# Kernel optimization log

Hardware: AMD Instinct MI355X
Metric: run time of the kernel (lower is better)

## Reference

```python
import jax, jax.numpy as jnp
import numpy as np

B, S, V, L, H, NH, NL = 4, 256, 64, 10, 128, 8, 3
DH = H // NH
LP1 = L + 1


def setup_inputs() -> dict:
    key = jax.random.key(0)
    ks = jax.random.split(key, 18)
    sc = 1.0 / np.sqrt(H)
    return {
        "x": jax.random.normal(ks[0], (B, S, V), jnp.float32),
        "adjacency_logits": jax.random.normal(ks[1], (V, V, LP1), jnp.float32) * 0.1,
        "var_emb": jax.random.normal(ks[2], (V, H), jnp.float32),
        "temp_emb": jax.random.normal(ks[3], (LP1, H), jnp.float32),
        "mech_W": jax.random.normal(ks[4], (V, NL, H, H), jnp.float32) * sc,
        "mech_b": jax.random.normal(ks[5], (V, NL, H), jnp.float32) * 0.01,
        "ln_g": jnp.ones((V, NL, H), jnp.float32),
        "ln_b": jnp.zeros((V, NL, H), jnp.float32),
        "Wq": jax.random.normal(ks[6], (V, H, H), jnp.float32) * sc,
        "Wk": jax.random.normal(ks[7], (V, H, H), jnp.float32) * sc,
        "Wv": jax.random.normal(ks[8], (V, H, H), jnp.float32) * sc,
        "Wo": jax.random.normal(ks[9], (V, H, H), jnp.float32) * sc,
        "bq": jnp.zeros((V, H), jnp.float32),
        "bk": jnp.zeros((V, H), jnp.float32),
        "bv": jnp.zeros((V, H), jnp.float32),
        "bo": jnp.zeros((V, H), jnp.float32),
        "out_W": jax.random.normal(ks[10], (V, H), jnp.float32) * sc,
        "out_b": jnp.zeros((V,), jnp.float32),
    }


def reference(x, adjacency_logits, var_emb, temp_emb, mech_W, mech_b, ln_g, ln_b,
              Wq, Wk, Wv, Wo, bq, bk, bv, bo, out_W, out_b):
    b, s, v = x.shape
    lp1 = adjacency_logits.shape[-1]
    adj = jax.nn.sigmoid(adjacency_logits)  # (V_src, V_tgt, L+1), soft adjacency

    # xlag[b,t,src,l] = x[b, t-l, src] with zero padding (the shift-pad loop, fused)
    xlag = jnp.stack([jnp.pad(x, ((0, 0), (l, 0), (0, 0)))[:, :s] for l in range(lp1)], axis=-1)

    # causal_input[b,t,tgt,h] = sum_{src,l} xlag * adj[src,tgt,l] * (var_emb[src,h] + temp_emb[l,h])
    A = jnp.einsum('btsl,sil->btis', xlag, adj)   # contracted over lag
    Bl = jnp.einsum('btsl,sil->btil', xlag, adj)  # contracted over source
    z = jnp.einsum('btis,sh->btih', A, var_emb) + jnp.einsum('btil,lh->btih', Bl, temp_emb)  # (B,S,V,H)

    # per-variable causal mechanism: Linear -> LayerNorm -> GELU (dropout = identity at eval)
    eps = 1e-5
    nl = mech_W.shape[1]
    for li in range(nl):
        z = jnp.einsum('btvh,vhk->btvk', z, mech_W[:, li]) + mech_b[:, li]
        mu = z.mean(axis=-1, keepdims=True)
        var = z.var(axis=-1, keepdims=True)
        z = (z - mu) / jnp.sqrt(var + eps) * ln_g[:, li] + ln_b[:, li]
        z = jax.nn.gelu(z, approximate=False)

    # per-variable multi-head self-attention over the sequence axis
    def heads(t):
        return t.reshape(b, s, v, NH, DH)
    q = heads(jnp.einsum('btvh,vhk->btvk', z, Wq) + bq)
    k = heads(jnp.einsum('btvh,vhk->btvk', z, Wk) + bk)
    vv = heads(jnp.einsum('btvh,vhk->btvk', z, Wv) + bv)
    scores = jnp.einsum('bqvnd,bkvnd->bvnqk', q, k) / np.sqrt(DH)  # (B,V,NH,S,S)
    attn = jax.nn.softmax(scores, axis=-1)
    o = jnp.einsum('bvnqk,bkvnd->bqvnd', attn, vv).reshape(b, s, v, NH * DH)
    o = jnp.einsum('btvh,vhk->btvk', o, Wo) + bo

    # per-variable output head Linear(H, 1), concatenated over variables
    predictions = jnp.einsum('btvh,vh->btv', o, out_W) + out_b  # (B,S,V)
    return predictions
```

## Files before the change

### kernel.cpp

```cpp
#include <hip/hip_runtime.h>
#include <math.h>

#define BB   4
#define SS   256
#define VV   64
#define LP1  11
#define HH   128
#define NHH  8
#define DHH  16
#define NLL  3
#define BSZ  1024

typedef unsigned short u16;
typedef unsigned int   u32;
typedef __attribute__((ext_vector_type(8))) short s16x8;
typedef __attribute__((ext_vector_type(4))) float f32x4;

__device__ __forceinline__ float bfbits2f(u32 hi16) {
    u32 i = hi16 << 16; float f; __builtin_memcpy(&f, &i, 4); return f;
}
__device__ __forceinline__ u16 f2bf(float f) {
    u32 i; __builtin_memcpy(&i, &f, 4);
    return (u16)((i + 0x7fffu + ((i >> 16) & 1u)) >> 16);
}
__device__ __forceinline__ u16 f2bf_trunc(float f) {
    u32 i; __builtin_memcpy(&i, &f, 4);
    return (u16)(i >> 16);
}
__device__ __forceinline__ float ldf(const void* p, size_t i, int isbf) {
    if (isbf) return bfbits2f(((const u16*)p)[i]);
    return ((const float*)p)[i];
}
__device__ __forceinline__ float4 ld4(const void* p, size_t i, int isbf) {
    float4 v;
    if (isbf) {
        uint2 u = *(const uint2*)((const u16*)p + i);
        v.x = bfbits2f(u.x & 0xffffu); v.y = bfbits2f(u.x >> 16);
        v.z = bfbits2f(u.y & 0xffffu); v.w = bfbits2f(u.y >> 16);
    } else {
        v = *(const float4*)((const float*)p + i);
    }
    return v;
}

__global__ __launch_bounds__(64) void k_sniff(const u16* __restrict__ probe,
                                              int* __restrict__ flags) {
    if (threadIdx.x == 0) {
        int wild = 0;
        for (int j = 0; j < 256; j++) {
            float v = bfbits2f(probe[j]);
            if (!(fabsf(v) < 1e8f)) wild = 1;
        }
        flags[0] = wild ? 0 : 1;
    }
}

__global__ __launch_bounds__(256) void k_adj(const void* __restrict__ logits,
                                             float* __restrict__ adj,
                                             const int* __restrict__ flags) {
    int isbf = flags[0];
    int i = blockIdx.x * 256 + threadIdx.x;
    if (i < VV * VV * LP1) {
        float v = ldf(logits, i, isbf);
        adj[i] = 1.f / (1.f + expf(-v));
    }
}

__global__ __launch_bounds__(128) void k_fuse(const void* __restrict__ Wo,
                                              const void* __restrict__ outW,
                                              const void* __restrict__ bo,
                                              const void* __restrict__ outb,
                                              float* __restrict__ wfused,
                                              float* __restrict__ bfused,
                                              const int* __restrict__ flags) {
    int isbf = flags[0];
    int v = blockIdx.x; int h = threadIdx.x;
    __shared__ float ow[HH];
    __shared__ float red[HH];
    ow[h] = ldf(outW, (size_t)v * HH + h, isbf);
    __syncthreads();
    size_t wb = ((size_t)v * HH + h) * HH;
    float acc = 0.f;
    #pragma unroll 8
    for (int k = 0; k < HH; k++) acc += ldf(Wo, wb + k, isbf) * ow[k];
    wfused[v * HH + h] = acc;
    red[h] = ldf(bo, (size_t)v * HH + h, isbf) * ow[h];
    __syncthreads();
    for (int s = 64; s > 0; s >>= 1) { if (h < s) red[h] += red[h + s]; __syncthreads(); }
    if (h == 0) bfused[v] = red[0] + ldf(outb, v, isbf);
}

__global__ __launch_bounds__(256) void k_causal(const void* __restrict__ x,
                                                const float* __restrict__ adj,
                                                const void* __restrict__ var_emb,
                                                const void* __restrict__ temp_emb,
                                                u16* __restrict__ zh,
                                                u16* __restrict__ zl,
                                                const int* __restrict__ flags) {
    __shared__ float xl[LP1][VV];
    __shared__ float A_sh[VV][VV + 1];
    __shared__ float Blp_sh[VV * LP1 * 4];
    __shared__ float Bl_sh[VV][12];
    int isbf = flags[0];
    int tid = threadIdx.x;
    int bt = blockIdx.x; int b = bt >> 8; int t = bt & 255;

    for (int p = tid; p < LP1 * VV; p += 256) {
        int l = p >> 6, s = p & 63; int tt = t - l;
        xl[l][s] = (tt >= 0) ? ldf(x, (size_t)(b * SS + tt) * VV + s, isbf) : 0.f;
    }
    __syncthreads();

    {
        int i = tid & 63, sg = tid >> 6;
        float blp[LP1];
        #pragma unroll
        for (int l = 0; l < LP1; l++) blp[l] = 0.f;
        for (int k = 0; k < 16; k++) {
            int s = sg + k * 4;
            const float* ap = adj + (s * VV + i) * LP1;
            float a = 0.f;
            #pragma unroll
            for (int l = 0; l < LP1; l++) {
                float pr = xl[l][s] * ap[l];
                a += pr; blp[l] += pr;
            }
            A_sh[i][s] = a;
        }
        #pragma unroll
        for (int l = 0; l < LP1; l++)
            Blp_sh[(i * LP1 + l) * 4 + sg] = blp[l];
    }
    __syncthreads();
    for (int p = tid; p < VV * LP1; p += 256) {
        int i = p / LP1, l = p - i * LP1;
        const float* q = &Blp_sh[(i * LP1 + l) * 4];
        Bl_sh[i][l] = (q[0] + q[1]) + (q[2] + q[3]);
    }
    __syncthreads();

    int h0 = (tid & 31) * 4;
    int ig = tid >> 5;
    float acc[8][4];
    #pragma unroll
    for (int ii = 0; ii < 8; ii++)
        #pragma unroll
        for (int j = 0; j < 4; j++) acc[ii][j] = 0.f;

    if (isbf) {
        for (int s = 0; s < VV; s++) {
            float4 v4 = ld4(var_emb, (size_t)s * HH + h0, 1);
            #pragma unroll
            for (int ii = 0; ii < 8; ii++) {
                float a = A_sh[ig * 8 + ii][s];
                acc[ii][0] += a * v4.x; acc[ii][1] += a * v4.y;
                acc[ii][2] += a * v4.z; acc[ii][3] += a * v4.w;
            }
        }
        #pragma unroll
        for (int l = 0; l < LP1; l++) {
            float4 t4 = ld4(temp_emb, (size_t)l * HH + h0, 1);
            #pragma unroll
            for (int ii = 0; ii < 8; ii++) {
                float bl = Bl_sh[ig * 8 + ii][l];
                acc[ii][0] += bl * t4.x; acc[ii][1] += bl * t4.y;
                acc[ii][2] += bl * t4.z; acc[ii][3] += bl * t4.w;
            }
        }
    } else {
        for (int s = 0; s < VV; s++) {
            float4 v4 = ld4(var_emb, (size_t)s * HH + h0, 0);
            #pragma unroll
            for (int ii = 0; ii < 8; ii++) {
                float a = A_sh[ig * 8 + ii][s];
                acc[ii][0] += a * v4.x; acc[ii][1] += a * v4.y;
                acc[ii][2] += a * v4.z; acc[ii][3] += a * v4.w;
            }
        }
        #pragma unroll
        for (int l = 0; l < LP1; l++) {
            float4 t4 = ld4(temp_emb, (size_t)l * HH + h0, 0);
            #pragma unroll
            for (int ii = 0; ii < 8; ii++) {
                float bl = Bl_sh[ig * 8 + ii][l];
                acc[ii][0] += bl * t4.x; acc[ii][1] += bl * t4.y;
                acc[ii][2] += bl * t4.z; acc[ii][3] += bl * t4.w;
            }
        }
    }

    #pragma unroll
    for (int ii = 0; ii < 8; ii++) {
        int i = ig * 8 + ii;
        size_t idx = ((size_t)i * BSZ + bt) * HH + h0;
        u16 h0_ = f2bf(acc[ii][0]), h1_ = f2bf(acc[ii][1]);
        u16 h2_ = f2bf(acc[ii][2]), h3_ = f2bf(acc[ii][3]);
        uint2 hw, lw;
        hw.x = (u32)h0_ | ((u32)h1_ << 16); hw.y = (u32)h2_ | ((u32)h3_ << 16);
        lw.x = (u32)f2bf(acc[ii][0] - bfbits2f(h0_)) | ((u32)f2bf(acc[ii][1] - bfbits2f(h1_)) << 16);
        lw.y = (u32)f2bf(acc[ii][2] - bfbits2f(h2_)) | ((u32)f2bf(acc[ii][3] - bfbits2f(h3_)) << 16);
        *(uint2*)&zh[idx] = hw;
        *(uint2*)&zl[idx] = lw;
    }
}

struct WPack {
    const void* src[4];
    u16* dh[4];
    u16* dl[4];
};
#define TP 136
__global__ __launch_bounds__(256) void k_wprep(WPack wp,
                                               const int* __restrict__ flags) {
    int isbf = flags[0];
    int mat = blockIdx.x;
    int seg = (mat < 192) ? 0 : 1 + ((mat - 192) >> 6);
    int rel = (mat < 192) ? mat : ((mat - 192) & 63);
    const void* raw = wp.src[seg];
    u16* Wh = wp.dh[seg];
    u16* Wl = wp.dl[seg];
    int tid = threadIdx.x;
    size_t src = (size_t)rel * (HH * HH);
    if (isbf) {
        __shared__ u16 tile[HH * TP];
        const uint4* sp = (const uint4*)((const u16*)raw + src);
        #pragma unroll
        for (int u = 0; u < 8; u++) {
            int p = u * 256 + tid;
            int h = p >> 4, k8 = (p & 15) * 8;
            int k8s = k8 ^ ((((u32)h >> 3) & 15) * 8);
            *(uint4*)&tile[h * TP + k8s] = sp[p];
        }
        __syncthreads();
        #pragma unroll
        for (int u = 0; u < 8; u++) {
            int p = u * 256 + tid;
            int kcol = p >> 4, h8 = (p & 15) * 8;
            u16 vals[8];
            #pragma unroll
            for (int j = 0; j < 8; j++) {
                int h = h8 + j;
                int ks = kcol ^ ((((u32)h >> 3) & 15) * 8);
                vals[j] = tile[h * TP + ks];
            }
            uint4 pk;
            pk.x = (u32)vals[0] | ((u32)vals[1] << 16);
            pk.y = (u32)vals[2] | ((u32)vals[3] << 16);
            pk.z = (u32)vals[4] | ((u32)vals[5] << 16);
            pk.w = (u32)vals[6] | ((u32)vals[7] << 16);
            *(uint4*)&Wh[src + (size_t)kcol * HH + h8] = pk;
        }
    } else {
        int kcol = tid >> 1, h0 = (tid & 1) * 64;
        size_t dst = src + (size_t)kcol * HH;
        for (int i = 0; i < 64; i++) {
            int h = h0 + i;
            float w = ldf(raw, src + (size_t)h * HH + kcol, 0);
            u16 hi = f2bf(w);
            Wh[dst + h] = hi;
            Wl[dst + h] = f2bf(w - bfbits2f(hi));
        }
    }
}

#define PZ 136
#define PB 72
__global__ __launch_bounds__(256) void k_mega(
    const u16* __restrict__ zh, const u16* __restrict__ zl,
    const u16* __restrict__ WmH, const u16* __restrict__ WmL,
    const u16* __restrict__ WqH, const u16* __restrict__ WqL,
    const u16* __restrict__ WkH, const u16* __restrict__ WkL,
    const u16* __restrict__ WvH, const u16* __restrict__ WvL,
    const void* __restrict__ mechb,
    const void* __restrict__ lng, const void* __restrict__ lnb,
    const void* __restrict__ bq, const void* __restrict__ bk,
    const void* __restrict__ bv,
    u16* __restrict__ Qh, u16* __restrict__ Ql,
    u16* __restrict__ Ko, u16* __restrict__ Vt,
    const int* __restrict__ flags)
{
    __shared__ u16 Az_h[64 * PZ];
    __shared__ u16 Az_l[64 * PZ];
    __shared__ u16 Bh_s[128 * PB];
    __shared__ u16 Bl_s[128 * PB];
    int isbf = flags[0];
    int wexact = isbf;
    int tid = threadIdx.x;
    int tile = blockIdx.x, v = blockIdx.y;
    int wave = tid >> 6, lane = tid & 63;
    int quad = lane >> 4, l15 = lane & 15;
    int m0 = wave * 16;

    size_t zbase = ((size_t)v * BSZ + (size_t)tile * 64) * HH;
    #pragma unroll
    for (int u = 0; u < 4; u++) {
        int idx = u * 256 + tid;
        int row = idx >> 4, k8 = (idx & 15) * 8;
        *(uint4*)&Az_h[row * PZ + k8] = *(const uint4*)&zh[zbase + (size_t)row * HH + k8];
        *(uint4*)&Az_l[row * PZ + k8] = *(const uint4*)&zl[zbase + (size_t)row * HH + k8];
    }

    for (int li = 0; li < 6; li++) {
        const u16* Wh; const u16* Wl; size_t wbase;
        if (li < 3)       { Wh = WmH; Wl = WmL; wbase = (size_t)(v * NLL + li) * (HH * HH); }
        else if (li == 3) { Wh = WqH; Wl = WqL; wbase = (size_t)v * (HH * HH); }
        else if (li == 4) { Wh = WkH; Wl = WkL; wbase = (size_t)v * (HH * HH); }
        else              { Wh = WvH; Wl = WvL; wbase = (size_t)v * (HH * HH); }

        f32x4 acc[8];
        #pragma unroll
        for (int nt = 0; nt < 8; nt++) {
            f32x4 zz = {0.f, 0.f, 0.f, 0.f};
            acc[nt] = zz;
        }

        for (int c = 0; c < 2; c++) {
            __syncthreads();
            #pragma unroll
            for (int u = 0; u < 4; u++) {
                int p = u * 256 + tid;
                int n = p >> 3, k8 = (p & 7) * 8;
                *(uint4*)&Bh_s[n * PB + k8] =
                    *(const uint4*)&Wh[wbase + (size_t)n * HH + c * 64 + k8];
            }
            if (!wexact) {
                #pragma unroll
                for (int u = 0; u < 4; u++) {
                    int p = u * 256 + tid;
                    int n = p >> 3, k8 = (p & 7) * 8;
                    *(uint4*)&Bl_s[n * PB + k8] =
                        *(const uint4*)&Wl[wbase + (size_t)n * HH + c * 64 + k8];
                }
            }
            __syncthreads();

            #pragma unroll
            for (int kk = 0; kk < 2; kk++) {
                int ka = c * 64 + kk * 32 + quad * 8;
                int kb = kk * 32 + quad * 8;
                s16x8 ah = *(const s16x8*)&Az_h[(m0 + l15) * PZ + ka];
                s16x8 al = *(const s16x8*)&Az_l[(m0 + l15) * PZ + ka];
                if (wexact) {
                    #pragma unroll
                    for (int nt = 0; nt < 8; nt++) {
                        s16x8 bh = *(const s16x8*)&Bh_s[(nt * 16 + l15) * PB + kb];
                        acc[nt] = __builtin_amdgcn_mfma_f32_16x16x32_bf16(ah, bh, acc[nt], 0, 0, 0);
                        acc[nt] = __builtin_amdgcn_mfma_f32_16x16x32_bf16(al, bh, acc[nt], 0, 0, 0);
                    }
                } else {
                    #pragma unroll
                    for (int nt = 0; nt < 8; nt++) {
                        s16x8 bh = *(const s16x8*)&Bh_s[(nt * 16 + l15) * PB + kb];
                        s16x8 bl = *(const s16x8*)&Bl_s[(nt * 16 + l15) * PB + kb];
                        acc[nt] = __builtin_amdgcn_mfma_f32_16x16x32_bf16(ah, bh, acc[nt], 0, 0, 0);
                        acc[nt] = __builtin_amdgcn_mfma_f32_16x16x32_bf16(al, bh, acc[nt], 0, 0, 0);
                        acc[nt] = __builtin_amdgcn_mfma_f32_16x16x32_bf16(ah, bl, acc[nt], 0, 0, 0);
                    }
                }
            }
        }

        float bcol[8], gcol[8], b2col[8];
        #pragma unroll
        for (int nt = 0; nt < 8; nt++) {
            int col = nt * 16 + l15;
            if (li < 3) {
                size_t pb = (size_t)v * (NLL * HH) + (size_t)li * HH + col;
                bcol[nt]  = ldf(mechb, pb, isbf);
                gcol[nt]  = ldf(lng, pb, isbf);
                b2col[nt] = ldf(lnb, pb, isbf);
            } else {
                const void* bp = (li == 3) ? bq : (li == 4) ? bk : bv;
                bcol[nt] = ldf(bp, (size_t)v * HH + col, isbf);
            }
        }
        #pragma unroll
        for (int r = 0; r < 4; r++) {
            float vals[8];
            float sum = 0.f, sq = 0.f;
            #pragma unroll
            for (int nt = 0; nt < 8; nt++) {
                float val = acc[nt][r] + bcol[nt];
                vals[nt] = val; sum += val; sq += val * val;
            }
            int rloc = m0 + quad * 4 + r;
            if (li < 3) {
                #pragma unroll
                for (int m = 1; m < 16; m <<= 1) {
                    sum += __shfl_xor(sum, m);
                    sq  += __shfl_xor(sq, m);
                }
                float mean = sum * (1.f / HH);
                float var  = sq * (1.f / HH) - mean * mean;
                float rstd = rsqrtf(var + 1e-5f);
                #pragma unroll
                for (int nt = 0; nt < 8; nt++) {
                    float y = (vals[nt] - mean) * rstd * gcol[nt] + b2col[nt];
                    y = 0.5f * y * (1.f + erff(y * 0.70710678118654752f));
                    u16 hi = f2bf(y);
                    Az_h[rloc * PZ + nt * 16 + l15] = hi;
                    Az_l[rloc * PZ + nt * 16 + l15] = f2bf(y - bfbits2f(hi));
                }
            } else {
                int row = tile * 64 + rloc;
                size_t ob = ((size_t)v * BSZ + row) * HH;
                if (li == 3) {
                    #pragma unroll
                    for (int nt = 0; nt < 8; nt++) {
                        u16 hi = f2bf(vals[nt]);
                        Qh[ob + nt * 16 + l15] = hi;
                        Ql[ob + nt * 16 + l15] = f2bf(vals[nt] - bfbits2f(hi));
                    }
                } else if (li == 4) {
                    #pragma unroll
                    for (int nt = 0; nt < 8; nt++)
                        Ko[ob + nt * 16 + l15] = f2bf(vals[nt]);
                } else {
                    int bb = row >> 8, tt = row & 255;
                    #pragma unroll
                    for (int nt = 0; nt < 8; nt++)
                        Vt[(((size_t)(v * BB + bb) * NHH + nt) * DHH + l15) * SS + tt] = f2bf(vals[nt]);
                }
            }
        }
    }
}

#define LDW 40
__global__ __launch_bounds__(256) void k_attn2(const u16* __restrict__ Qh,
                                               const u16* __restrict__ Ql,
                                               const u16* __restrict__ K16,
                                               const u16* __restrict__ Vt,
                                               float* __restrict__ O) {
    __shared__ u16 Kp_sh[SS * LDW];
    __shared__ u16 Vt_sh[DHH * 264];
    __shared__ u16 P_sh[4][16 * LDW];
    int tid = threadIdx.x;
    int wave = tid >> 6, lane = tid & 63;
    int quad = lane >> 4, l15 = lane & 15;
    int bn = blockIdx.x, v = blockIdx.y;
    int b = bn >> 3, n = bn & 7;
    size_t qkbase = ((size_t)v * BSZ + b * SS) * HH + n * DHH;
    size_t vtbase = ((size_t)(v * BB + b) * NHH + n) * DHH * SS;

    {
        int row = tid;
        uint4 k0 = *(const uint4*)&K16[qkbase + (size_t)row * HH];
        uint4 k1 = *(const uint4*)&K16[qkbase + (size_t)row * HH + 8];
        *(uint4*)&Kp_sh[row * LDW + 0]  = k0;
        *(uint4*)&Kp_sh[row * LDW + 8]  = k1;
        *(uint4*)&Kp_sh[row * LDW + 16] = k0;
        *(uint4*)&Kp_sh[row * LDW + 24] = k1;
    }
    #pragma unroll
    for (int u = 0; u < 2; u++) {
        int p = u * 256 + tid;
        int d = p >> 5, su = (p & 31) * 8;
        *(uint4*)&Vt_sh[d * 264 + su] = *(const uint4*)&Vt[vtbase + (size_t)d * SS + su];
    }
    __syncthreads();

    s16x8 ones;
    #pragma unroll
    for (int i = 0; i < 8; i++) ones[i] = (short)0x3F80;

    for (int mt = wave * 4; mt < wave * 4 + 4; mt++) {
        const u16* Qsrc = (quad < 2) ? Qh : Ql;
        s16x8 aq = *(const s16x8*)&Qsrc[qkbase + (size_t)(mt * 16 + l15) * HH + (quad & 1) * 8];
        f32x4 oacc = {0.f, 0.f, 0.f, 0.f};
        f32x4 lacc = {0.f, 0.f, 0.f, 0.f};
        for (int jt2 = 0; jt2 < 8; jt2++) {
            #pragma unroll
            for (int sub = 0; sub < 2; sub++) {
                int jt = jt2 * 2 + sub;
                s16x8 bk = *(const s16x8*)&Kp_sh[(jt * 16 + l15) * LDW + quad * 8];
                f32x4 s = {0.f, 0.f, 0.f, 0.f};
                s = __builtin_amdgcn_mfma_f32_16x16x32_bf16(aq, bk, s, 0, 0, 0);
                #pragma unroll
                for (int r = 0; r < 4; r++) {
                    float p = __expf(s[r] * 0.25f);
                    P_sh[wave][(quad * 4 + r) * LDW + sub * 16 + l15] = f2bf_trunc(p);
                }
            }
            s16x8 ap = *(const s16x8*)&P_sh[wave][l15 * LDW + quad * 8];
            s16x8 bv = *(const s16x8*)&Vt_sh[l15 * 264 + jt2 * 32 + quad * 8];
            oacc = __builtin_amdgcn_mfma_f32_16x16x32_bf16(ap, bv, oacc, 0, 0, 0);
            lacc = __builtin_amdgcn_mfma_f32_16x16x32_bf16(ap, ones, lacc, 0, 0, 0);
        }
        #pragma unroll
        for (int r = 0; r < 4; r++) {
            float val = oacc[r] / lacc[r];
            O[((size_t)v * BSZ + b * SS + mt * 16 + quad * 4 + r) * HH + n * DHH + l15] = val;
        }
    }
}

__global__ __launch_bounds__(256) void k_final(const float* __restrict__ o,
                                               const float* __restrict__ wfused,
                                               const float* __restrict__ bfused,
                                               void* __restrict__ out,
                                               const int* __restrict__ flags) {
    __shared__ float wf[HH];
    int isbf = flags[0];
    int tid = threadIdx.x; int b = blockIdx.x; int v = blockIdx.y;
    if (tid < HH) wf[tid] = wfused[v * HH + tid];
    __syncthreads();
    int rg = tid >> 3;
    int l8 = tid & 7;
    float4 w0 = *(const float4*)&wf[l8 * 16];
    float4 w1 = *(const float4*)&wf[l8 * 16 + 4];
    float4 w2 = *(const float4*)&wf[l8 * 16 + 8];
    float4 w3 = *(const float4*)&wf[l8 * 16 + 12];
    float bv = bfused[v];
    #pragma unroll
    for (int pass = 0; pass < 8; pass++) {
        int bt = b * SS + pass * 32 + rg;
        const float4* orow = (const float4*)(o + ((size_t)v * BSZ + bt) * HH + l8 * 16);
        float4 a0 = orow[0], a1 = orow[1], a2 = orow[2], a3 = orow[3];
        float acc = a0.x * w0.x + a0.y * w0.y + a0.z * w0.z + a0.w * w0.w
                  + a1.x * w1.x + a1.y * w1.y + a1.z * w1.z + a1.w * w1.w
                  + a2.x * w2.x + a2.y * w2.y + a2.z * w2.z + a2.w * w2.w
                  + a3.x * w3.x + a3.y * w3.y + a3.z * w3.z + a3.w * w3.w;
        acc += __shfl_xor(acc, 1);
        acc += __shfl_xor(acc, 2);
        acc += __shfl_xor(acc, 4);
        if (l8 == 0) {
            float pred = acc + bv;
            size_t oi = (size_t)bt * VV + v;
            if (isbf) ((u16*)out)[oi] = f2bf(pred);
            else      ((float*)out)[oi] = pred;
        }
    }
}

extern "C" void kernel_launch(void* const* d_in, const int* in_sizes, int n_in,
                              void* d_out, int out_size, void* d_ws, size_t ws_size,
                              hipStream_t stream) {
    (void)out_size; (void)ws_size;

    static const int dict_sizes[18]  = {65536,45056,8192,1408,3145728,24576,24576,24576,
                                        1048576,1048576,1048576,1048576,8192,8192,8192,8192,8192,64};
    static const int alpha_sizes[18] = {1048576,1048576,1048576,1048576,45056,8192,8192,8192,
                                        8192,24576,24576,3145728,24576,8192,64,1408,8192,65536};
    static const int alpha_pos[18]   = {17,4,16,15,11,12,10,9,2,0,3,1,7,5,8,6,13,14};
    static const int alpha_logical[18] = {9,11,8,10,1,13,15,12,14,7,6,4,5,16,17,3,2,0};

    const void* in[18];
    bool is_dict = (n_in == 18), is_alpha = (n_in == 18);
    for (int i = 0; i < 18 && i < n_in; i++) {
        if (in_sizes[i] != dict_sizes[i])  is_dict = false;
        if (in_sizes[i] != alpha_sizes[i]) is_alpha = false;
    }
    if (is_dict) {
        for (int i = 0; i < 18; i++) in[i] = d_in[i];
    } else if (is_alpha) {
        for (int i = 0; i < 18; i++) in[i] = d_in[alpha_pos[i]];
    } else {
        bool used[18] = {false};
        for (int a = 0; a < 18; a++) {
            int lg = alpha_logical[a];
            for (int i = 0; i < n_in && i < 18; i++) {
                if (!used[i] && in_sizes[i] == dict_sizes[lg]) {
                    in[lg] = d_in[i]; used[i] = true; break;
                }
            }
        }
    }

    const void* x        = in[0];
    const void* adjl     = in[1];
    const void* var_emb  = in[2];
    const void* temp_emb = in[3];
    const void* mechW    = in[4];
    const void* mechb    = in[5];
    const void* lng      = in[6];
    const void* lnb      = in[7];
    const void* Wq       = in[8];
    const void* Wk       = in[9];
    const void* Wv       = in[10];
    const void* Wo       = in[11];
    const void* bq       = in[12];
    const void* bk       = in[13];
    const void* bv       = in[14];
    const void* bo       = in[15];
    const void* outW     = in[16];
    const void* outb     = in[17];

    float* ws     = (float*)d_ws;
    int*   flags  = (int*)ws;
    float* adj    = ws + 32;
    float* wfused = ws + 45088;
    float* bfused = ws + 53280;
    u16*   zhA    = (u16*)(ws + 53376);
    u16*   zlA    = (u16*)(ws + 4247680);
    u16*   zhB    = (u16*)(ws + 8441984);
    u16*   zlB    = (u16*)(ws + 12636288);
    float* Obuf   = ws + 53376;
    u16*   K16    = (u16*)(ws + 16830592);
    u16*   Vt16   = (u16*)(ws + 21024896);
    u16*   WtmH   = (u16*)(ws + 25219200);
    u16*   WtmL   = (u16*)(ws + 26792064);
    u16*   WtqH   = (u16*)(ws + 28364928);
    u16*   WtqL   = (u16*)(ws + 28889216);
    u16*   WtkH   = (u16*)(ws + 29413504);
    u16*   WtkL   = (u16*)(ws + 29937792);
    u16*   WtvH   = (u16*)(ws + 30462080);
    u16*   WtvL   = (u16*)(ws + 30986368);

    k_sniff <<<dim3(1),    dim3(64),  0, stream>>>((const u16*)mechW, flags);
    k_adj   <<<dim3(176),  dim3(256), 0, stream>>>(adjl, adj, flags);
    k_fuse  <<<dim3(64),   dim3(128), 0, stream>>>(Wo, outW, bo, outb, wfused, bfused, flags);
    k_causal<<<dim3(BSZ),  dim3(256), 0, stream>>>(x, adj, var_emb, temp_emb, zhA, zlA, flags);

    WPack wp;
    wp.src[0] = mechW; wp.dh[0] = WtmH; wp.dl[0] = WtmL;
    wp.src[1] = Wq;    wp.dh[1] = WtqH; wp.dl[1] = WtqL;
    wp.src[2] = Wk;    wp.dh[2] = WtkH; wp.dl[2] = WtkL;
    wp.src[3] = Wv;    wp.dh[3] = WtvH; wp.dl[3] = WtvL;
    k_wprep <<<dim3(384),  dim3(256), 0, stream>>>(wp, flags);

    k_mega<<<dim3(16, 64), dim3(256), 0, stream>>>(
            zhA, zlA,
            WtmH, WtmL, WtqH, WtqL, WtkH, WtkL, WtvH, WtvL,
            mechb, lng, lnb, bq, bk, bv,
            zhB, zlB, K16, Vt16, flags);

    k_attn2 <<<dim3(BB * NHH, VV), dim3(256), 0, stream>>>(zhB, zlB, K16, Vt16, Obuf);
    k_final <<<dim3(BB, VV), dim3(256), 0, stream>>>(Obuf, wfused, bfused, d_out, flags);
}
```

Measured before the change: 399.7 us.

## Pipeline weight chunk loads through registers and stage V transpose in k_mega

Restructures the fused MLP/QKV kernel so the weight tiles stream as chunks, with the next chunk prefetched into registers while the MFMAs run on the current one. The separate low-part weight buffer is removed from shared memory, and the hi/lo weight parts become separate chunks. The V output is transposed through shared memory so the global writes are coalesced 16-byte stores. The grid is flattened with an XCD-aware block-to-variable mapping, and launch bounds request 3 blocks per CU. The risks are higher register pressure from the prefetch buffers and more barriers per layer.

```diff
diff --git a/kernel.cpp b/kernel.cpp
--- a/kernel.cpp
+++ b/kernel.cpp
@@ -263,9 +263,9 @@
     }
 }
 
-#define PZ 136
-#define PB 72
-__global__ __launch_bounds__(256) void k_mega(
+#define PZq 136
+#define PB  72
+__global__ __launch_bounds__(256, 3) void k_mega(
     const u16* __restrict__ zh, const u16* __restrict__ zl,
     const u16* __restrict__ WmH, const u16* __restrict__ WmL,
     const u16* __restrict__ WqH, const u16* __restrict__ WqL,
@@ -279,14 +279,17 @@
     u16* __restrict__ Ko, u16* __restrict__ Vt,
     const int* __restrict__ flags)
 {
-    __shared__ u16 Az_h[64 * PZ];
-    __shared__ u16 Az_l[64 * PZ];
+    __shared__ u16 Az_h[64 * PZq];
+    __shared__ u16 Az_l[64 * PZq];
     __shared__ u16 Bh_s[128 * PB];
-    __shared__ u16 Bl_s[128 * PB];
+    u16* Vt_sh = Bh_s;
     int isbf = flags[0];
     int wexact = isbf;
     int tid = threadIdx.x;
-    int tile = blockIdx.x, v = blockIdx.y;
+    int bid = blockIdx.x;
+    int xcd = bid & 7, idx = bid >> 3;
+    int v = xcd * 8 + (idx >> 4);
+    int tile = idx & 15;
     int wave = tid >> 6, lane = tid & 63;
     int quad = lane >> 4, l15 = lane & 15;
     int m0 = wave * 16;
@@ -294,72 +297,34 @@
     size_t zbase = ((size_t)v * BSZ + (size_t)tile * 64) * HH;
     #pragma unroll
     for (int u = 0; u < 4; u++) {
-        int idx = u * 256 + tid;
-        int row = idx >> 4, k8 = (idx & 15) * 8;
-        *(uint4*)&Az_h[row * PZ + k8] = *(const uint4*)&zh[zbase + (size_t)row * HH + k8];
-        *(uint4*)&Az_l[row * PZ + k8] = *(const uint4*)&zl[zbase + (size_t)row * HH + k8];
-    }
-
-    for (int li = 0; li < 6; li++) {
-        const u16* Wh; const u16* Wl; size_t wbase;
-        if (li < 3)       { Wh = WmH; Wl = WmL; wbase = (size_t)(v * NLL + li) * (HH * HH); }
-        else if (li == 3) { Wh = WqH; Wl = WqL; wbase = (size_t)v * (HH * HH); }
-        else if (li == 4) { Wh = WkH; Wl = WkL; wbase = (size_t)v * (HH * HH); }
-        else              { Wh = WvH; Wl = WvL; wbase = (size_t)v * (HH * HH); }
-
-        f32x4 acc[8];
-        #pragma unroll
-        for (int nt = 0; nt < 8; nt++) {
-            f32x4 zz = {0.f, 0.f, 0.f, 0.f};
-            acc[nt] = zz;
-        }
-
-        for (int c = 0; c < 2; c++) {
-            __syncthreads();
-            #pragma unroll
-            for (int u = 0; u < 4; u++) {
-                int p = u * 256 + tid;
-                int n = p >> 3, k8 = (p & 7) * 8;
-                *(uint4*)&Bh_s[n * PB + k8] =
-                    *(const uint4*)&Wh[wbase + (size_t)n * HH + c * 64 + k8];
-            }
-            if (!wexact) {
-                #pragma unroll
-                for (int u = 0; u < 4; u++) {
-                    int p = u * 256 + tid;
-                    int n = p >> 3, k8 = (p & 7) * 8;
-                    *(uint4*)&Bl_s[n * PB + k8] =
-                        *(const uint4*)&Wl[wbase + (size_t)n * HH + c * 64 + k8];
-                }
-            }
-            __syncthreads();
-
-            #pragma unroll
-            for (int kk = 0; kk < 2; kk++) {
-                int ka = c * 64 + kk * 32 + quad * 8;
-                int kb = kk * 32 + quad * 8;
-                s16x8 ah = *(const s16x8*)&Az_h[(m0 + l15) * PZ + ka];
-                s16x8 al = *(const s16x8*)&Az_l[(m0 + l15) * PZ + ka];
-                if (wexact) {
-                    #pragma unroll
-                    for (int nt = 0; nt < 8; nt++) {
-                        s16x8 bh = *(const s16x8*)&Bh_s[(nt * 16 + l15) * PB + kb];
-                        acc[nt] = __builtin_amdgcn_mfma_f32_16x16x32_bf16(ah, bh, acc[nt], 0, 0, 0);
-                        acc[nt] = __builtin_amdgcn_mfma_f32_16x16x32_bf16(al, bh, acc[nt], 0, 0, 0);
-                    }
-                } else {
-                    #pragma unroll
-                    for (int nt = 0; nt < 8; nt++) {
-                        s16x8 bh = *(const s16x8*)&Bh_s[(nt * 16 + l15) * PB + kb];
-                        s16x8 bl = *(const s16x8*)&Bl_s[(nt * 16 + l15) * PB + kb];
-                        acc[nt] = __builtin_amdgcn_mfma_f32_16x16x32_bf16(ah, bh, acc[nt], 0, 0, 0);
-                        acc[nt] = __builtin_amdgcn_mfma_f32_16x16x32_bf16(al, bh, acc[nt], 0, 0, 0);
-                        acc[nt] = __builtin_amdgcn_mfma_f32_16x16x32_bf16(ah, bl, acc[nt], 0, 0, 0);
-                    }
-                }
-            }
-        }
-
+        int p = u * 256 + tid;
+        int row = p >> 4, k8 = (p & 15) * 8;
+        *(uint4*)&Az_h[row * PZq + k8] = *(const uint4*)&zh[zbase + (size_t)row * HH + k8];
+        *(uint4*)&Az_l[row * PZq + k8] = *(const uint4*)&zl[zbase + (size_t)row * HH + k8];
+    }
+
+    int shift = wexact ? 1 : 2;
+    int PER = 1 << shift;
+    int NCH = 6 << shift;
+    int n0 = tid >> 3;
+    int k8u = (tid & 7) * 8;
+
+    auto wsrc = [&](int ch) -> const u16* {
+        int li = ch >> shift;
+        int sub = ch & (PER - 1);
+        int cc = sub & 1;
+        int lo = sub >> 1;
+        const u16* p; size_t wb;
+        if (li < 3)       { p = lo ? WmL : WmH; wb = (size_t)(v * NLL + li) * (HH * HH); }
+        else if (li == 3) { p = lo ? WqL : WqH; wb = (size_t)v * (HH * HH); }
+        else if (li == 4) { p = lo ? WkL : WkH; wb = (size_t)v * (HH * HH); }
+        else              { p = lo ? WvL : WvH; wb = (size_t)v * (HH * HH); }
+        return p + wb + cc * 64;
+    };
+
+    f32x4 acc[8];
+
+    auto epilogue = [&](int li) {
         float bcol[8], gcol[8], b2col[8];
         #pragma unroll
         for (int nt = 0; nt < 8; nt++) {
@@ -374,6 +339,7 @@
                 bcol[nt] = ldf(bp, (size_t)v * HH + col, isbf);
             }
         }
+        if (li == 5) __syncthreads();
         #pragma unroll
         for (int r = 0; r < 4; r++) {
             float vals[8];
@@ -398,32 +364,106 @@
                     float y = (vals[nt] - mean) * rstd * gcol[nt] + b2col[nt];
                     y = 0.5f * y * (1.f + erff(y * 0.70710678118654752f));
                     u16 hi = f2bf(y);
-                    Az_h[rloc * PZ + nt * 16 + l15] = hi;
-                    Az_l[rloc * PZ + nt * 16 + l15] = f2bf(y - bfbits2f(hi));
+                    Az_h[rloc * PZq + nt * 16 + l15] = hi;
+                    Az_l[rloc * PZq + nt * 16 + l15] = f2bf(y - bfbits2f(hi));
                 }
-            } else {
+            } else if (li == 3) {
                 int row = tile * 64 + rloc;
                 size_t ob = ((size_t)v * BSZ + row) * HH;
-                if (li == 3) {
-                    #pragma unroll
-                    for (int nt = 0; nt < 8; nt++) {
-                        u16 hi = f2bf(vals[nt]);
-                        Qh[ob + nt * 16 + l15] = hi;
-                        Ql[ob + nt * 16 + l15] = f2bf(vals[nt] - bfbits2f(hi));
-                    }
-                } else if (li == 4) {
-                    #pragma unroll
-                    for (int nt = 0; nt < 8; nt++)
-                        Ko[ob + nt * 16 + l15] = f2bf(vals[nt]);
-                } else {
-                    int bb = row >> 8, tt = row & 255;
-                    #pragma unroll
-                    for (int nt = 0; nt < 8; nt++)
-                        Vt[(((size_t)(v * BB + bb) * NHH + nt) * DHH + l15) * SS + tt] = f2bf(vals[nt]);
+                #pragma unroll
+                for (int nt = 0; nt < 8; nt++) {
+                    u16 hi = f2bf(vals[nt]);
+                    Qh[ob + nt * 16 + l15] = hi;
+                    Ql[ob + nt * 16 + l15] = f2bf(vals[nt] - bfbits2f(hi));
                 }
-            }
-        }
-    }
+            } else if (li == 4) {
+                int row = tile * 64 + rloc;
+                size_t ob = ((size_t)v * BSZ + row) * HH;
+                #pragma unroll
+                for (int nt = 0; nt < 8; nt++)
+                    Ko[ob + nt * 16 + l15] = f2bf(vals[nt]);
+            } else {
+                #pragma unroll
+                for (int nt = 0; nt < 8; nt++)
+                    Vt_sh[(nt * 16 + l15) * PB + rloc] = f2bf(vals[nt]);
+            }
+        }
+        if (li == 5) {
+            __syncthreads();
+            int col = tid >> 1, half = tid & 1;
+            int n = col >> 4, d = col & 15;
+            int bb = tile >> 2, t0 = (tile & 3) * 64;
+            size_t dst = (((size_t)(v * BB + bb) * NHH + n) * DHH + d) * SS + t0 + half * 32;
+            #pragma unroll
+            for (int j = 0; j < 4; j++)
+                *(uint4*)&Vt[dst + j * 8] = *(const uint4*)&Vt_sh[col * PB + half * 32 + j * 8];
+        }
+    };
+
+#define MEGA_STEP(CH, STG, PRF)                                              \
+  {                                                                          \
+    int ch_ = (CH);                                                          \
+    __syncthreads();   \
+    _Pragma("unroll")                                                        \
+    for (int u = 0; u < 4; u++)                                              \
+        *(uint4*)&Bh_s[(u * 32 + n0) * PB + k8u] = STG[u];                   \
+    if (ch_ + 1 < NCH) {                                                     \
+        const u16* s_ = wsrc(ch_ + 1);                                       \
+        _Pragma("unroll")                                                    \
+        for (int u = 0; u < 4; u++)                                          \
+            PRF[u] = *(const uint4*)&s_[(size_t)(u * 32 + n0) * HH + k8u];   \
+    }                                                                        \
+     \
+    asm volatile("s_waitcnt lgkmcnt(0)" ::: "memory");                       \
+    __builtin_amdgcn_s_barrier();                                            \
+    {                                                                        \
+        int sub_ = ch_ & (PER - 1);                                          \
+        int li_ = ch_ >> shift;                                              \
+        int cc_ = sub_ & 1, lo_ = sub_ >> 1;                                 \
+        if (sub_ == 0) {                                                     \
+            _Pragma("unroll")                                                \
+            for (int nt = 0; nt < 8; nt++) {                                 \
+                f32x4 zz = {0.f, 0.f, 0.f, 0.f};                             \
+                acc[nt] = zz;                                                \
+            }                                                                \
+        }                                                                    \
+        _Pragma("unroll")                                                    \
+        for (int kk = 0; kk < 2; kk++) {                                     \
+            int ka = cc_ * 64 + kk * 32 + quad * 8;                          \
+            int kb = kk * 32 + quad * 8;                                     \
+            s16x8 ah = *(const s16x8*)&Az_h[(m0 + l15) * PZq + ka];          \
+            if (!lo_) {                                                      \
+                s16x8 al = *(const s16x8*)&Az_l[(m0 + l15) * PZq + ka];      \
+                _Pragma("unroll")                                            \
+                for (int nt = 0; nt < 8; nt++) {                             \
+                    s16x8 bh = *(const s16x8*)&Bh_s[(nt * 16 + l15) * PB + kb]; \
+                    acc[nt] = __builtin_amdgcn_mfma_f32_16x16x32_bf16(ah, bh, acc[nt], 0, 0, 0); \
+                    acc[nt] = __builtin_amdgcn_mfma_f32_16x16x32_bf16(al, bh, acc[nt], 0, 0, 0); \
+                }                                                            \
+            } else {                                                         \
+                _Pragma("unroll")                                            \
+                for (int nt = 0; nt < 8; nt++) {                             \
+                    s16x8 bl = *(const s16x8*)&Bh_s[(nt * 16 + l15) * PB + kb]; \
+                    acc[nt] = __builtin_amdgcn_mfma_f32_16x16x32_bf16(ah, bl, acc[nt], 0, 0, 0); \
+                }                                                            \
+            }                                                                \
+        }                                                                    \
+        if (sub_ == PER - 1) epilogue(li_);                                  \
+    }                                                                        \
+  }
+
+    uint4 pa[4], pb[4];
+    {
+        const u16* s0 = wsrc(0);
+        #pragma unroll
+        for (int u = 0; u < 4; u++)
+            pa[u] = *(const uint4*)&s0[(size_t)(u * 32 + n0) * HH + k8u];
+    }
+    for (int ch = 0; ch < NCH; ch += 2) {
+        MEGA_STEP(ch, pa, pb);
+        MEGA_STEP(ch + 1, pb, pa);
+    }
+#undef MEGA_STEP
 }
 
 #define LDW 40
@@ -619,7 +659,7 @@
     wp.src[3] = Wv;    wp.dh[3] = WtvH; wp.dl[3] = WtvL;
     k_wprep <<<dim3(384),  dim3(256), 0, stream>>>(wp, flags);
 
-    k_mega<<<dim3(16, 64), dim3(256), 0, stream>>>(
+    k_mega<<<dim3(1024), dim3(256), 0, stream>>>(
             zhA, zlA,
             WtmH, WtmL, WtqH, WtqL, WtkH, WtkL, WtvH, WtvL,
             mechb, lng, lnb, bq, bk, bv,
```

New measurement: 482.1 us. +20.6%, slower.

## Double-buffer weight chunks via global_load_lds with swizzled LDS and XCD-aware block mapping

Applied to the files above, without the earlier changes.

Restructures k_mega so each weight chunk (hi/lo halves, 64-wide K blocks) is staged into a double-buffered LDS tile with direct global-to-LDS loads while the previous chunk is consumed by MFMAs. Weights are pre-laid-out by k_wprep in an XOR-swizzled chunked format, and activations now use an unpadded XOR-swizzled LDS layout instead of padding. Blocks are remapped so the tiles of one variable land on the same XCD to improve L2 reuse of weights, and the V-transpose output is staged through LDS for coalesced stores. The aim is to hide weight-load latency and cut LDS bank conflicts, at the cost of more barriers per layer and reliance on the swizzle matching between prep and consumer.

```diff
diff --git a/kernel.cpp b/kernel.cpp
--- a/kernel.cpp
+++ b/kernel.cpp
@@ -41,6 +41,11 @@
         v = *(const float4*)((const float*)p + i);
     }
     return v;
+}
+__device__ __forceinline__ void gll16(const u16* g, u16* l) {
+    __builtin_amdgcn_global_load_lds(
+        (const __attribute__((address_space(1))) void*)g,
+        (__attribute__((address_space(3))) void*)l, 16, 0, 0);
 }
 
 __global__ __launch_bounds__(64) void k_sniff(const u16* __restrict__ probe,
@@ -248,23 +253,25 @@
             pk.y = (u32)vals[2] | ((u32)vals[3] << 16);
             pk.z = (u32)vals[4] | ((u32)vals[5] << 16);
             pk.w = (u32)vals[6] | ((u32)vals[7] << 16);
-            *(uint4*)&Wh[src + (size_t)kcol * HH + h8] = pk;
+            int c = h8 >> 6;
+            int kloc = (h8 & 63) ^ ((kcol & 7) * 8);
+            *(uint4*)&Wh[src + c * 8192 + kcol * 64 + kloc] = pk;
         }
     } else {
         int kcol = tid >> 1, h0 = (tid & 1) * 64;
-        size_t dst = src + (size_t)kcol * HH;
         for (int i = 0; i < 64; i++) {
             int h = h0 + i;
             float w = ldf(raw, src + (size_t)h * HH + kcol, 0);
             u16 hi = f2bf(w);
-            Wh[dst + h] = hi;
-            Wl[dst + h] = f2bf(w - bfbits2f(hi));
-        }
-    }
-}
-
-#define PZ 136
-#define PB 72
+            int c = h >> 6;
+            size_t dst = src + c * 8192 + (size_t)kcol * 64 + ((h & 63) ^ ((kcol & 7) * 8));
+            Wh[dst] = hi;
+            Wl[dst] = f2bf(w - bfbits2f(hi));
+        }
+    }
+}
+
+#define PB  72
 __global__ __launch_bounds__(256) void k_mega(
     const u16* __restrict__ zh, const u16* __restrict__ zl,
     const u16* __restrict__ WmH, const u16* __restrict__ WmL,
@@ -279,87 +286,64 @@
     u16* __restrict__ Ko, u16* __restrict__ Vt,
     const int* __restrict__ flags)
 {
-    __shared__ u16 Az_h[64 * PZ];
-    __shared__ u16 Az_l[64 * PZ];
-    __shared__ u16 Bh_s[128 * PB];
-    __shared__ u16 Bl_s[128 * PB];
+    __shared__ u16 Az_h[64 * 128];
+    __shared__ u16 Az_l[64 * 128];
+    __shared__ u16 Bd_s[2][128 * 64];
+    u16* Vt_sh = &Bd_s[0][0];
     int isbf = flags[0];
     int wexact = isbf;
     int tid = threadIdx.x;
-    int tile = blockIdx.x, v = blockIdx.y;
+    int bid = blockIdx.x;
+    int xcd = bid & 7, idx = bid >> 3;
+    int v = xcd * 8 + (idx >> 4);
+    int tile = idx & 15;
     int wave = tid >> 6, lane = tid & 63;
     int quad = lane >> 4, l15 = lane & 15;
     int m0 = wave * 16;
+    int swzl = (l15 & 7) * 8;
 
     size_t zbase = ((size_t)v * BSZ + (size_t)tile * 64) * HH;
-    #pragma unroll
-    for (int u = 0; u < 4; u++) {
-        int idx = u * 256 + tid;
-        int row = idx >> 4, k8 = (idx & 15) * 8;
-        *(uint4*)&Az_h[row * PZ + k8] = *(const uint4*)&zh[zbase + (size_t)row * HH + k8];
-        *(uint4*)&Az_l[row * PZ + k8] = *(const uint4*)&zl[zbase + (size_t)row * HH + k8];
-    }
-
-    for (int li = 0; li < 6; li++) {
-        const u16* Wh; const u16* Wl; size_t wbase;
-        if (li < 3)       { Wh = WmH; Wl = WmL; wbase = (size_t)(v * NLL + li) * (HH * HH); }
-        else if (li == 3) { Wh = WqH; Wl = WqL; wbase = (size_t)v * (HH * HH); }
-        else if (li == 4) { Wh = WkH; Wl = WkL; wbase = (size_t)v * (HH * HH); }
-        else              { Wh = WvH; Wl = WvL; wbase = (size_t)v * (HH * HH); }
-
-        f32x4 acc[8];
-        #pragma unroll
-        for (int nt = 0; nt < 8; nt++) {
-            f32x4 zz = {0.f, 0.f, 0.f, 0.f};
-            acc[nt] = zz;
-        }
-
-        for (int c = 0; c < 2; c++) {
-            __syncthreads();
-            #pragma unroll
-            for (int u = 0; u < 4; u++) {
-                int p = u * 256 + tid;
-                int n = p >> 3, k8 = (p & 7) * 8;
-                *(uint4*)&Bh_s[n * PB + k8] =
-                    *(const uint4*)&Wh[wbase + (size_t)n * HH + c * 64 + k8];
-            }
-            if (!wexact) {
-                #pragma unroll
-                for (int u = 0; u < 4; u++) {
-                    int p = u * 256 + tid;
-                    int n = p >> 3, k8 = (p & 7) * 8;
-                    *(uint4*)&Bl_s[n * PB + k8] =
-                        *(const uint4*)&Wl[wbase + (size_t)n * HH + c * 64 + k8];
-                }
-            }
-            __syncthreads();
-
-            #pragma unroll
-            for (int kk = 0; kk < 2; kk++) {
-                int ka = c * 64 + kk * 32 + quad * 8;
-                int kb = kk * 32 + quad * 8;
-                s16x8 ah = *(const s16x8*)&Az_h[(m0 + l15) * PZ + ka];
-                s16x8 al = *(const s16x8*)&Az_l[(m0 + l15) * PZ + ka];
-                if (wexact) {
-                    #pragma unroll
-                    for (int nt = 0; nt < 8; nt++) {
-                        s16x8 bh = *(const s16x8*)&Bh_s[(nt * 16 + l15) * PB + kb];
-                        acc[nt] = __builtin_amdgcn_mfma_f32_16x16x32_bf16(ah, bh, acc[nt], 0, 0, 0);
-                        acc[nt] = __builtin_amdgcn_mfma_f32_16x16x32_bf16(al, bh, acc[nt], 0, 0, 0);
-                    }
-                } else {
-                    #pragma unroll
-                    for (int nt = 0; nt < 8; nt++) {
-                        s16x8 bh = *(const s16x8*)&Bh_s[(nt * 16 + l15) * PB + kb];
-                        s16x8 bl = *(const s16x8*)&Bl_s[(nt * 16 + l15) * PB + kb];
-                        acc[nt] = __builtin_amdgcn_mfma_f32_16x16x32_bf16(ah, bh, acc[nt], 0, 0, 0);
-                        acc[nt] = __builtin_amdgcn_mfma_f32_16x16x32_bf16(al, bh, acc[nt], 0, 0, 0);
-                        acc[nt] = __builtin_amdgcn_mfma_f32_16x16x32_bf16(ah, bl, acc[nt], 0, 0, 0);
-                    }
-                }
-            }
-        }
-
+
+    int shift = wexact ? 1 : 2;
+    int PER = 1 << shift;
+    int NCH = 6 << shift;
+
+    auto wchunk = [&](int ch) -> const u16* {
+        int li = ch >> shift;
+        int sub = ch & (PER - 1);
+        int cc = sub & 1, lo = sub >> 1;
+        const u16* p; size_t wb;
+        if (li < 3)       { p = lo ? WmL : WmH; wb = (size_t)(v * NLL + li) * 16384; }
+        else if (li == 3) { p = lo ? WqL : WqH; wb = (size_t)v * 16384; }
+        else if (li == 4) { p = lo ? WkL : WkH; wb = (size_t)v * 16384; }
+        else              { p = lo ? WvL : WvH; wb = (size_t)v * 16384; }
+        return p + wb + cc * 8192;
+    };
+    auto stageB = [&](u16* dst, const u16* g) {
+        const u16* gl = g + wave * 2048 + lane * 8;
+        u16* lb = dst + wave * 2048;
+        #pragma unroll
+        for (int u = 0; u < 4; u++)
+            gll16(gl + u * 512, lb + u * 512);
+    };
+
+    {
+        int rl = lane >> 4;
+        int kc = (lane & 15) * 8;
+        #pragma unroll
+        for (int u = 0; u < 4; u++) {
+            int row = wave * 16 + u * 4 + rl;
+            int kcs = kc ^ ((row & 7) * 8);
+            gll16(&zh[zbase + (size_t)row * HH + kcs], &Az_h[(wave * 16 + u * 4) * 128]);
+            gll16(&zl[zbase + (size_t)row * HH + kcs], &Az_l[(wave * 16 + u * 4) * 128]);
+        }
+    }
+    stageB(&Bd_s[0][0], wchunk(0));
+    __syncthreads();
+
+    f32x4 acc[8];
+
+    auto epilogue = [&](int li) {
         float bcol[8], gcol[8], b2col[8];
         #pragma unroll
         for (int nt = 0; nt < 8; nt++) {
@@ -374,6 +358,7 @@
                 bcol[nt] = ldf(bp, (size_t)v * HH + col, isbf);
             }
         }
+        if (li == 5) __syncthreads();
         #pragma unroll
         for (int r = 0; r < 4; r++) {
             float vals[8];
@@ -393,36 +378,86 @@
                 float mean = sum * (1.f / HH);
                 float var  = sq * (1.f / HH) - mean * mean;
                 float rstd = rsqrtf(var + 1e-5f);
+                int swr = (rloc & 7) * 8;
                 #pragma unroll
                 for (int nt = 0; nt < 8; nt++) {
                     float y = (vals[nt] - mean) * rstd * gcol[nt] + b2col[nt];
                     y = 0.5f * y * (1.f + erff(y * 0.70710678118654752f));
                     u16 hi = f2bf(y);
-                    Az_h[rloc * PZ + nt * 16 + l15] = hi;
-                    Az_l[rloc * PZ + nt * 16 + l15] = f2bf(y - bfbits2f(hi));
+                    int colw = (nt * 16 + l15) ^ swr;
+                    Az_h[rloc * 128 + colw] = hi;
+                    Az_l[rloc * 128 + colw] = f2bf(y - bfbits2f(hi));
+                }
+            } else if (li == 3) {
+                int row = tile * 64 + rloc;
+                size_t ob = ((size_t)v * BSZ + row) * HH;
+                #pragma unroll
+                for (int nt = 0; nt < 8; nt++) {
+                    u16 hi = f2bf(vals[nt]);
+                    Qh[ob + nt * 16 + l15] = hi;
+                    Ql[ob + nt * 16 + l15] = f2bf(vals[nt] - bfbits2f(hi));
+                }
+            } else if (li == 4) {
+                int row = tile * 64 + rloc;
+                size_t ob = ((size_t)v * BSZ + row) * HH;
+                #pragma unroll
+                for (int nt = 0; nt < 8; nt++)
+                    Ko[ob + nt * 16 + l15] = f2bf(vals[nt]);
+            } else {
+                #pragma unroll
+                for (int nt = 0; nt < 8; nt++)
+                    Vt_sh[(nt * 16 + l15) * PB + rloc] = f2bf(vals[nt]);
+            }
+        }
+        if (li == 5) {
+            __syncthreads();
+            int col = tid >> 1, half = tid & 1;
+            int n = col >> 4, d = col & 15;
+            int bb = tile >> 2, t0 = (tile & 3) * 64;
+            size_t dst = (((size_t)(v * BB + bb) * NHH + n) * DHH + d) * SS + t0 + half * 32;
+            #pragma unroll
+            for (int j = 0; j < 4; j++)
+                *(uint4*)&Vt[dst + j * 8] = *(const uint4*)&Vt_sh[col * PB + half * 32 + j * 8];
+        }
+    };
+
+    for (int ch = 0; ch < NCH; ch++) {
+        int bsel = ch & 1;
+        if (ch + 1 < NCH) stageB(&Bd_s[bsel ^ 1][0], wchunk(ch + 1));
+        int sub = ch & (PER - 1);
+        int li = ch >> shift;
+        int cc = sub & 1, lo = sub >> 1;
+        if (sub == 0) {
+            #pragma unroll
+            for (int nt = 0; nt < 8; nt++) {
+                f32x4 zz = {0.f, 0.f, 0.f, 0.f};
+                acc[nt] = zz;
+            }
+        }
+        const u16* Bp = &Bd_s[bsel][0];
+        #pragma unroll
+        for (int kk = 0; kk < 2; kk++) {
+            int acol = (cc * 64 + kk * 32 + quad * 8) ^ swzl;
+            int bcol = (kk * 32 + quad * 8) ^ swzl;
+            s16x8 ah = *(const s16x8*)&Az_h[(m0 + l15) * 128 + acol];
+            if (!lo) {
+                s16x8 al = *(const s16x8*)&Az_l[(m0 + l15) * 128 + acol];
+                #pragma unroll
+                for (int nt = 0; nt < 8; nt++) {
+                    s16x8 bh = *(const s16x8*)&Bp[(nt * 16 + l15) * 64 + bcol];
+                    acc[nt] = __builtin_amdgcn_mfma_f32_16x16x32_bf16(ah, bh, acc[nt], 0, 0, 0);
+                    acc[nt] = __builtin_amdgcn_mfma_f32_16x16x32_bf16(al, bh, acc[nt], 0, 0, 0);
                 }
             } else {
-                int row = tile * 64 + rloc;
-                size_t ob = ((size_t)v * BSZ + row) * HH;
-                if (li == 3) {
-                    #pragma unroll
-                    for (int nt = 0; nt < 8; nt++) {
-                        u16 hi = f2bf(vals[nt]);
-                        Qh[ob + nt * 16 + l15] = hi;
-                        Ql[ob + nt * 16 + l15] = f2bf(vals[nt] - bfbits2f(hi));
-                    }
-                } else if (li == 4) {
-                    #pragma unroll
-                    for (int nt = 0; nt < 8; nt++)
-                        Ko[ob + nt * 16 + l15] = f2bf(vals[nt]);
-                } else {
-                    int bb = row >> 8, tt = row & 255;
-                    #pragma unroll
-                    for (int nt = 0; nt < 8; nt++)
-                        Vt[(((size_t)(v * BB + bb) * NHH + nt) * DHH + l15) * SS + tt] = f2bf(vals[nt]);
+                #pragma unroll
+                for (int nt = 0; nt < 8; nt++) {
+                    s16x8 bl = *(const s16x8*)&Bp[(nt * 16 + l15) * 64 + bcol];
+                    acc[nt] = __builtin_amdgcn_mfma_f32_16x16x32_bf16(ah, bl, acc[nt], 0, 0, 0);
                 }
             }
         }
+        if (sub == PER - 1) epilogue(li);
+        __syncthreads();
     }
 }
 
@@ -610,7 +645,6 @@
     k_sniff <<<dim3(1),    dim3(64),  0, stream>>>((const u16*)mechW, flags);
     k_adj   <<<dim3(176),  dim3(256), 0, stream>>>(adjl, adj, flags);
     k_fuse  <<<dim3(64),   dim3(128), 0, stream>>>(Wo, outW, bo, outb, wfused, bfused, flags);
-    k_causal<<<dim3(BSZ),  dim3(256), 0, stream>>>(x, adj, var_emb, temp_emb, zhA, zlA, flags);
 
     WPack wp;
     wp.src[0] = mechW; wp.dh[0] = WtmH; wp.dl[0] = WtmL;
@@ -619,7 +653,9 @@
     wp.src[3] = Wv;    wp.dh[3] = WtvH; wp.dl[3] = WtvL;
     k_wprep <<<dim3(384),  dim3(256), 0, stream>>>(wp, flags);
 
-    k_mega<<<dim3(16, 64), dim3(256), 0, stream>>>(
+    k_causal<<<dim3(BSZ),  dim3(256), 0, stream>>>(x, adj, var_emb, temp_emb, zhA, zlA, flags);
+
+    k_mega<<<dim3(1024), dim3(256), 0, stream>>>(
             zhA, zlA,
             WtmH, WtmL, WtqH, WtqL, WtkH, WtkL, WtvH, WtvL,
             mechb, lng, lnb, bq, bk, bv,
```

Result: slower. 420.5 us (+5.2%).
